# Kernel optimization log

Hardware: AMD Instinct MI355X
Metric: run time of the kernel (lower is better)

## Reference

```python
import jax, jax.numpy as jnp
import numpy as np

N_HEADS = 4
D_K = 32
C = 128
SCALE = D_K ** (-0.5)


def setup_inputs() -> dict:
    key = jax.random.key(0)
    k1, k2, k3, k4, k5 = jax.random.split(key, 5)
    x = jax.random.normal(k1, (16, C, 32, 32), dtype=jnp.float32)
    # nn.Linear(C, n_heads*d_k*3): weight [out, in], bias [out]
    Wp = jax.random.normal(k2, (N_HEADS * D_K * 3, C), dtype=jnp.float32) * (C ** -0.5)
    bp = jax.random.normal(k3, (N_HEADS * D_K * 3,), dtype=jnp.float32) * 0.01
    # nn.Linear(n_heads*d_k, C)
    Wo = jax.random.normal(k4, (C, N_HEADS * D_K), dtype=jnp.float32) * ((N_HEADS * D_K) ** -0.5)
    bo = jax.random.normal(k5, (C,), dtype=jnp.float32) * 0.01
    return {"x": x, "Wp": Wp, "bp": bp, "Wo": Wo, "bo": bo}


def reference(x, Wp, bp, Wo, bo):
    b, c, h, w = x.shape
    n = h * w
    # (b,c,h,w) -> (b, n, c); NOTE: GroupNorm from __init__ is never applied in forward.
    xf = x.reshape(b, c, n).transpose(0, 2, 1)
    qkv = (xf @ Wp.T + bp).reshape(b, n, N_HEADS, 3 * D_K)
    q, k, v = jnp.split(qkv, 3, axis=-1)  # each (b, n, heads, d_k)
    attn = jnp.einsum('bihd,bjhd->bijh', q, k) * SCALE  # (b, n, n, heads)
    # Faithful to original: softmax over LAST axis = heads axis (original code bug)
    attn = jax.nn.softmax(attn, axis=-1)
    res = jnp.einsum('bijh,bjhd->bihd', attn, v).reshape(b, n, N_HEADS * D_K)
    res = res @ Wo.T + bo + xf
    return res.transpose(0, 2, 1).reshape(b, c, h, w)
```

## Files before the change

### kernel.cpp

```cpp
#include <hip/hip_runtime.h>

typedef short s8v __attribute__((ext_vector_type(8)));
typedef float f4v __attribute__((ext_vector_type(4)));

#define NTOK 1024
#define CD 128
#define QSCALE 0.25506953149031838f

__device__ __forceinline__ ushort f2bf(float x) {
    union { float f; unsigned u; } v; v.f = x;
    unsigned u = v.u + 0x7fff + ((v.u >> 16) & 1);
    return (ushort)(u >> 16);
}
__device__ __forceinline__ float bf2f(ushort x) {
    union { unsigned u; float f; } v; v.u = ((unsigned)x) << 16;
    return v.f;
}
__device__ __forceinline__ void gl_lds16(const ushort* g, ushort* l) {
    __builtin_amdgcn_global_load_lds(
        (const __attribute__((address_space(1))) unsigned int*)(g),
        (__attribute__((address_space(3))) unsigned int*)(l), 16, 0, 0);
}
__device__ __forceinline__ unsigned cvt_pk_bf16(float lo, float hi) {
    unsigned r;
    asm("v_cvt_pk_bf16_f32 %0, %1, %2" : "=v"(r) : "v"(lo), "v"(hi));
    return r;
}

__global__ __launch_bounds__(256) void k_pre(const float* __restrict__ x,
                                             const float* __restrict__ Wp,
                                             const float* __restrict__ Wo,
                                             ushort* __restrict__ xt,
                                             ushort* __restrict__ wpre) {
    const int t = threadIdx.x;
    const int bx = blockIdx.x;
    if (bx < 256) {
        __shared__ ushort tile[128 * 68];
        const int b = bx >> 4;
        const int n0 = (bx & 15) << 6;
        #pragma unroll
        for (int p = 0; p < 8; ++p) {
            const int c = p * 16 + (t >> 4);
            const int n4 = t & 15;
            const float4 v = *(const float4*)&x[(b * CD + c) * NTOK + n0 + n4 * 4];
            ushort4 o;
            o.x = f2bf(v.x); o.y = f2bf(v.y); o.z = f2bf(v.z); o.w = f2bf(v.w);
            *(ushort4*)&tile[c * 68 + n4 * 4] = o;
        }
        __syncthreads();
        #pragma unroll
        for (int p = 0; p < 4; ++p) {
            const int nl = t >> 2;
            const int g = (t & 3) + p * 4;
            s8v tmp;
            #pragma unroll
            for (int e = 0; e < 8; ++e) tmp[e] = (short)tile[(g * 8 + e) * 68 + nl];
            const int n = n0 + nl;
            *(s8v*)&xt[(b * NTOK + n) * CD + ((g ^ (nl & 7)) * 8)] = tmp;
        }
    } else {
        const int kind = bx - 256;
        ushort* dst = wpre + kind * (CD * CD);
        for (int e = t * 4; e < CD * CD; e += 1024) {
            const int f = e >> 7, c = e & 127;
            const float* src;
            if (kind == 3) src = &Wo[f * CD + c];
            else           src = &Wp[((f >> 5) * 96 + kind * 32 + (f & 31)) * CD + c];
            const float4 v = *(const float4*)src;
            ushort4 o;
            o.x = f2bf(v.x); o.y = f2bf(v.y); o.z = f2bf(v.z); o.w = f2bf(v.w);
            *(ushort4*)&dst[f * CD + (((c >> 3) ^ (f & 7)) * 8) + (c & 7)] = o;
        }
    }
}

__global__ __launch_bounds__(256) void k_proj(const ushort* __restrict__ xt,
                                              const ushort* __restrict__ wpre,
                                              const float* __restrict__ bp,
                                              ushort* __restrict__ qb,
                                              ushort* __restrict__ kb,
                                              ushort* __restrict__ vtb) {
    __shared__ ushort Abuf[128 * 128];
    __shared__ ushort Bbuf[64 * 128];
    const int t = threadIdx.x;
    const int lane = t & 63;
    const int w = t >> 6;
    const int li = lane & 15;
    const int lg = lane >> 4;
    const int bx = blockIdx.x;
    const int kind = bx >> 8;
    const int idx = bx & 255;

    const ushort* Asrc;
    const ushort* Bsrc;
    if (kind < 2) {
        Asrc = xt + (idx >> 1) * 128 * CD;
        Bsrc = wpre + kind * (CD * CD) + (idx & 1) * 64 * CD;
    } else {
        Asrc = wpre + 2 * (CD * CD);
        Bsrc = xt + idx * 64 * CD;
    }
    {
        const ushort* ga = Asrc + w * 4096;
        ushort* la = Abuf + w * 4096;
        #pragma unroll
        for (int i = 0; i < 8; ++i) gl_lds16(ga + i * 512 + lane * 8, la + i * 512);
        const ushort* gb = Bsrc + w * 2048;
        ushort* lb = Bbuf + w * 2048;
        #pragma unroll
        for (int i = 0; i < 4; ++i) gl_lds16(gb + i * 512 + lane * 8, lb + i * 512);
    }
    __syncthreads();

    const f4v fz = {0.f, 0.f, 0.f, 0.f};
    f4v acc[2][4];
    #pragma unroll
    for (int mf = 0; mf < 2; ++mf)
        #pragma unroll
        for (int nf = 0; nf < 4; ++nf) acc[mf][nf] = fz;
    const int m_base = w * 32;
    #pragma unroll
    for (int kk = 0; kk < 4; ++kk) {
        s8v a[2], bb[4];
        #pragma unroll
        for (int mf = 0; mf < 2; ++mf) {
            const int row = m_base + mf * 16 + li;
            a[mf] = *(const s8v*)&Abuf[row * CD + (((kk * 4 + lg) ^ (row & 7)) * 8)];
        }
        #pragma unroll
        for (int nf = 0; nf < 4; ++nf) {
            const int row = nf * 16 + li;
            bb[nf] = *(const s8v*)&Bbuf[row * CD + (((kk * 4 + lg) ^ (row & 7)) * 8)];
        }
        #pragma unroll
        for (int mf = 0; mf < 2; ++mf)
            #pragma unroll
            for (int nf = 0; nf < 4; ++nf)
                acc[mf][nf] = __builtin_amdgcn_mfma_f32_16x16x32_bf16(a[mf], bb[nf], acc[mf][nf], 0, 0, 0);
    }

    if (kind < 2) {
        ushort* dst = (kind == 0) ? qb : kb;
        const int m0 = (idx >> 1) * 128;
        const int f0 = (idx & 1) * 64;
        #pragma unroll
        for (int mf = 0; mf < 2; ++mf)
            #pragma unroll
            for (int nf = 0; nf < 4; ++nf) {
                const int f = f0 + nf * 16 + li;
                const int o = (f >> 5) * 96 + kind * 32 + (f & 31);
                const float bias = bp[o];
                #pragma unroll
                for (int r = 0; r < 4; ++r) {
                    const int row = m0 + m_base + mf * 16 + lg * 4 + r;
                    float v = acc[mf][nf][r] + bias;
                    if (kind == 0) v *= QSCALE;
                    dst[row * CD + f] = f2bf(v);
                }
            }
    } else {
        const int n0g = idx * 64;
        const int b = n0g >> 10;
        const int nl0 = n0g & 1023;
        #pragma unroll
        for (int mf = 0; mf < 2; ++mf)
            #pragma unroll
            for (int r = 0; r < 4; ++r) {
                const int f = m_base + mf * 16 + lg * 4 + r;
                const int o = (f >> 5) * 96 + 64 + (f & 31);
                const float bias = bp[o];
                #pragma unroll
                for (int nf = 0; nf < 4; ++nf) {
                    const int n = nl0 + nf * 16 + li;
                    const int jl = n & 31;
                    const int np = (n & ~31) | (((jl & 15) >> 2) * 8 + (jl & 3) + ((jl >> 4) << 2));
                    vtb[(b * CD + f) * NTOK + np] = f2bf(acc[mf][nf][r] + bias);
                }
            }
    }
}

__global__ __launch_bounds__(256) void k_attn(const ushort* __restrict__ qb,
                                              const ushort* __restrict__ kb,
                                              const ushort* __restrict__ vtb,
                                              ushort* __restrict__ res4) {
    __shared__ ushort kbuf[2][32 * 136];
    __shared__ ushort vbuf[2][128 * 40];
    const int t = threadIdx.x;
    const int lane = t & 63;
    const int w = t >> 6;
    const int b = blockIdx.x;
    const int it = blockIdx.y;
    const int js = blockIdx.z;
    const int i0 = it * 64 + w * 16;
    const int li = lane & 15;
    const int lg = lane >> 4;

    s8v qf[4];
    #pragma unroll
    for (int h = 0; h < 4; ++h)
        qf[h] = *(const s8v*)&qb[(b*NTOK + i0 + li)*CD + h*32 + lg*8];

    const f4v fz = {0.f, 0.f, 0.f, 0.f};
    f4v acc[4][2];
    #pragma unroll
    for (int h = 0; h < 4; ++h) { acc[h][0] = fz; acc[h][1] = fz; }

    const int j0 = js * 256;
    const ushort* kptr0 = &kb[(b*NTOK + j0 + (t>>4))*CD + (t&15)*8];
    const ushort* kptr1 = kptr0 + 16*CD;
    const ushort* vptr0 = &vtb[(b*CD + (t>>2))*NTOK + j0 + (t&3)*8];
    const ushort* vptr1 = vptr0 + 64*NTOK;
    const int kwo = (t>>4)*136 + (t&15)*8;
    const int vwo = (t>>2)*40 + (t&3)*8;

    s8v k0 = *(const s8v*)kptr0;
    s8v k1 = *(const s8v*)kptr1;
    s8v v0 = *(const s8v*)vptr0;
    s8v v1 = *(const s8v*)vptr1;
    *(s8v*)&kbuf[0][kwo]          = k0;
    *(s8v*)&kbuf[0][kwo + 16*136] = k1;
    *(s8v*)&vbuf[0][vwo]          = v0;
    *(s8v*)&vbuf[0][vwo + 64*40]  = v1;
    k0 = *(const s8v*)(kptr0 + 32*CD);
    k1 = *(const s8v*)(kptr1 + 32*CD);
    v0 = *(const s8v*)(vptr0 + 32);
    v1 = *(const s8v*)(vptr1 + 32);
    __syncthreads();

    unsigned wv[4][4];
    {
        f4v sv[4][2];
        __builtin_amdgcn_s_setprio(1);
        #pragma unroll
        for (int h = 0; h < 4; ++h)
            #pragma unroll
            for (int jh = 0; jh < 2; ++jh) {
                s8v kf = *(const s8v*)&kbuf[0][(jh*16 + li)*136 + h*32 + lg*8];
                sv[h][jh] = __builtin_amdgcn_mfma_f32_16x16x32_bf16(kf, qf[h], fz, 0, 0, 0);
            }
        __builtin_amdgcn_s_setprio(0);
        #pragma unroll
        for (int jh = 0; jh < 2; ++jh)
            #pragma unroll
            for (int r = 0; r < 4; ++r) {
                float e0 = __builtin_amdgcn_exp2f(sv[0][jh][r]);
                float e1 = __builtin_amdgcn_exp2f(sv[1][jh][r]);
                float e2 = __builtin_amdgcn_exp2f(sv[2][jh][r]);
                float e3 = __builtin_amdgcn_exp2f(sv[3][jh][r]);
                float inv = __builtin_amdgcn_rcpf(e0 + e1 + e2 + e3);
                sv[0][jh][r] = e0 * inv;
                sv[1][jh][r] = e1 * inv;
                sv[2][jh][r] = e2 * inv;
                sv[3][jh][r] = e3 * inv;
            }
        #pragma unroll
        for (int h = 0; h < 4; ++h) {
            wv[h][0] = cvt_pk_bf16(sv[h][0][0], sv[h][0][1]);
            wv[h][1] = cvt_pk_bf16(sv[h][0][2], sv[h][0][3]);
            wv[h][2] = cvt_pk_bf16(sv[h][1][0], sv[h][1][1]);
            wv[h][3] = cvt_pk_bf16(sv[h][1][2], sv[h][1][3]);
        }
    }

    #pragma unroll
    for (int tt = 1; tt <= 8; ++tt) {
        if (tt <= 7) {
            ushort* kn = kbuf[tt & 1];
            *(s8v*)&kn[kwo]          = k0;
            *(s8v*)&kn[kwo + 16*136] = k1;
        }
        __syncthreads();
        if (tt <= 7) {
            ushort* vn = vbuf[tt & 1];
            *(s8v*)&vn[vwo]          = v0;
            *(s8v*)&vn[vwo + 64*40]  = v1;
        }
        if (tt <= 6) {
            k0 = *(const s8v*)(kptr0 + (tt+1)*32*CD);
            k1 = *(const s8v*)(kptr1 + (tt+1)*32*CD);
            v0 = *(const s8v*)(vptr0 + (tt+1)*32);
            v1 = *(const s8v*)(vptr1 + (tt+1)*32);
        }
        f4v sv[4][2];
        if (tt <= 7) {
            const ushort* kc = kbuf[tt & 1];
            __builtin_amdgcn_s_setprio(1);
            #pragma unroll
            for (int h = 0; h < 4; ++h)
                #pragma unroll
                for (int jh = 0; jh < 2; ++jh) {
                    s8v kf = *(const s8v*)&kc[(jh*16 + li)*136 + h*32 + lg*8];
                    sv[h][jh] = __builtin_amdgcn_mfma_f32_16x16x32_bf16(kf, qf[h], fz, 0, 0, 0);
                }
            __builtin_amdgcn_s_setprio(0);
        }
        {
            const ushort* vc = vbuf[(tt - 1) & 1];
            #pragma unroll
            for (int h = 0; h < 4; ++h) {
                union { unsigned d[4]; s8v s; } av;
                av.d[0] = wv[h][0]; av.d[1] = wv[h][1];
                av.d[2] = wv[h][2]; av.d[3] = wv[h][3];
                s8v vf0 = *(const s8v*)&vc[(h*32 + li)*40 + lg*8];
                s8v vf1 = *(const s8v*)&vc[(h*32 + 16 + li)*40 + lg*8];
                __builtin_amdgcn_s_setprio(1);
                acc[h][0] = __builtin_amdgcn_mfma_f32_16x16x32_bf16(av.s, vf0, acc[h][0], 0, 0, 0);
                acc[h][1] = __builtin_amdgcn_mfma_f32_16x16x32_bf16(av.s, vf1, acc[h][1], 0, 0, 0);
                __builtin_amdgcn_s_setprio(0);
            }
        }
        if (tt <= 7) {
            #pragma unroll
            for (int jh = 0; jh < 2; ++jh)
                #pragma unroll
                for (int r = 0; r < 4; ++r) {
                    float e0 = __builtin_amdgcn_exp2f(sv[0][jh][r]);
                    float e1 = __builtin_amdgcn_exp2f(sv[1][jh][r]);
                    float e2 = __builtin_amdgcn_exp2f(sv[2][jh][r]);
                    float e3 = __builtin_amdgcn_exp2f(sv[3][jh][r]);
                    float inv = __builtin_amdgcn_rcpf(e0 + e1 + e2 + e3);
                    sv[0][jh][r] = e0 * inv;
                    sv[1][jh][r] = e1 * inv;
                    sv[2][jh][r] = e2 * inv;
                    sv[3][jh][r] = e3 * inv;
                }
            #pragma unroll
            for (int h = 0; h < 4; ++h) {
                wv[h][0] = cvt_pk_bf16(sv[h][0][0], sv[h][0][1]);
                wv[h][1] = cvt_pk_bf16(sv[h][0][2], sv[h][0][3]);
                wv[h][2] = cvt_pk_bf16(sv[h][1][0], sv[h][1][1]);
                wv[h][3] = cvt_pk_bf16(sv[h][1][2], sv[h][1][3]);
            }
        }
    }

    #pragma unroll
    for (int h = 0; h < 4; ++h)
        #pragma unroll
        for (int dh = 0; dh < 2; ++dh)
            #pragma unroll
            for (int r = 0; r < 4; ++r) {
                const int i = i0 + lg*4 + r;
                const int f = h*32 + dh*16 + li;
                res4[js*(16*NTOK*CD) + (b*NTOK + i)*CD + f] = f2bf(acc[h][dh][r]);
            }
}

__global__ __launch_bounds__(256) void k_out(const ushort* __restrict__ wpre,
                                             const ushort* __restrict__ res4,
                                             const float* __restrict__ bo,
                                             const float* __restrict__ x,
                                             float* __restrict__ out) {
    __shared__ ushort Abuf[128 * 128];
    __shared__ ushort Bbuf[64 * 128];
    const int t = threadIdx.x;
    const int lane = t & 63;
    const int w = t >> 6;
    const int li = lane & 15;
    const int lg = lane >> 4;
    const int idx = blockIdx.x;
    const int n0g = idx * 64;
    const int b = n0g >> 10;
    {
        const ushort* ga = wpre + 3 * (CD * CD) + w * 4096;
        ushort* la = Abuf + w * 4096;
        #pragma unroll
        for (int i = 0; i < 8; ++i) gl_lds16(ga + i * 512 + lane * 8, la + i * 512);
    }
    for (int u = t; u < 64 * 16; u += 256) {
        const int rl = u >> 4, g = u & 15;
        const ushort* p = &res4[(n0g + rl) * CD + g * 8];
        s8v p0 = *(const s8v*)(p);
        s8v p1 = *(const s8v*)(p + 16*NTOK*CD);
        s8v p2 = *(const s8v*)(p + 32*NTOK*CD);
        s8v p3 = *(const s8v*)(p + 48*NTOK*CD);
        s8v sm;
        #pragma unroll
        for (int e = 0; e < 8; ++e)
            sm[e] = (short)f2bf(bf2f((ushort)p0[e]) + bf2f((ushort)p1[e])
                              + bf2f((ushort)p2[e]) + bf2f((ushort)p3[e]));
        *(s8v*)&Bbuf[rl * CD + ((g ^ (rl & 7)) * 8)] = sm;
    }
    __syncthreads();

    const f4v fz = {0.f, 0.f, 0.f, 0.f};
    f4v acc[2][4];
    #pragma unroll
    for (int mf = 0; mf < 2; ++mf)
        #pragma unroll
        for (int nf = 0; nf < 4; ++nf) acc[mf][nf] = fz;
    const int m_base = w * 32;
    #pragma unroll
    for (int kk = 0; kk < 4; ++kk) {
        s8v a[2], bb[4];
        #pragma unroll
        for (int mf = 0; mf < 2; ++mf) {
            const int row = m_base + mf * 16 + li;
            a[mf] = *(const s8v*)&Abuf[row * CD + (((kk * 4 + lg) ^ (row & 7)) * 8)];
        }
        #pragma unroll
        for (int nf = 0; nf < 4; ++nf) {
            const int row = nf * 16 + li;
            bb[nf] = *(const s8v*)&Bbuf[row * CD + (((kk * 4 + lg) ^ (row & 7)) * 8)];
        }
        #pragma unroll
        for (int mf = 0; mf < 2; ++mf)
            #pragma unroll
            for (int nf = 0; nf < 4; ++nf)
                acc[mf][nf] = __builtin_amdgcn_mfma_f32_16x16x32_bf16(a[mf], bb[nf], acc[mf][nf], 0, 0, 0);
    }
    const int nl0 = n0g & 1023;
    #pragma unroll
    for (int mf = 0; mf < 2; ++mf)
        #pragma unroll
        for (int r = 0; r < 4; ++r) {
            const int o = m_base + mf * 16 + lg * 4 + r;
            const float bias = bo[o];
            #pragma unroll
            for (int nf = 0; nf < 4; ++nf) {
                const int n = nl0 + nf * 16 + li;
                const int gi = (b * CD + o) * NTOK + n;
                out[gi] = acc[mf][nf][r] + bias + x[gi];
            }
        }
}

extern "C" void kernel_launch(void* const* d_in, const int* in_sizes, int n_in,
                              void* d_out, int out_size, void* d_ws, size_t ws_size,
                              hipStream_t stream) {
    const float* x  = (const float*)d_in[0];
    const float* Wp = (const float*)d_in[1];
    const float* bp = (const float*)d_in[2];
    const float* Wo = (const float*)d_in[3];
    const float* bo = (const float*)d_in[4];
    float* out = (float*)d_out;
    ushort* xt   = (ushort*)d_ws;
    ushort* wpre = xt + 16*1024*128;
    ushort* qbw  = wpre + 4*128*128;
    ushort* kbw  = qbw + 16*1024*128;
    ushort* vtb  = kbw + 16*1024*128;
    ushort* res4 = vtb + 16*1024*128;
    k_pre <<<260, 256, 0, stream>>>(x, Wp, Wo, xt, wpre);
    k_proj<<<768, 256, 0, stream>>>(xt, wpre, bp, qbw, kbw, vtb);
    k_attn<<<dim3(16, 16, 4), 256, 0, stream>>>(qbw, kbw, vtb, res4);
    k_out <<<256, 256, 0, stream>>>(wpre, res4, bo, x, out);
}
```

Baseline: 49.34 us.

## Widen projection tiles to full feature width and double attention block size

The Q/K projection blocks now compute all 128 output features per 128-token tile, so each block loads the x tile once instead of two blocks each loading it. The grid shrinks from 768 to 512 blocks. The attention kernel moves to 512-thread blocks covering 128 query rows, so each K/V tile staged in shared memory is shared by twice as many query rows and each thread loads half as much. This trades fewer blocks and more registers and LDS per block for less redundant global traffic.

```diff
diff --git a/kernel.cpp b/kernel.cpp
--- a/kernel.cpp
+++ b/kernel.cpp
@@ -81,73 +81,64 @@
                                               ushort* __restrict__ kb,
                                               ushort* __restrict__ vtb) {
     __shared__ ushort Abuf[128 * 128];
-    __shared__ ushort Bbuf[64 * 128];
+    __shared__ ushort Bbuf[128 * 128];
     const int t = threadIdx.x;
     const int lane = t & 63;
     const int w = t >> 6;
     const int li = lane & 15;
     const int lg = lane >> 4;
     const int bx = blockIdx.x;
-    const int kind = bx >> 8;
-    const int idx = bx & 255;
-
-    const ushort* Asrc;
-    const ushort* Bsrc;
-    if (kind < 2) {
-        Asrc = xt + (idx >> 1) * 128 * CD;
-        Bsrc = wpre + kind * (CD * CD) + (idx & 1) * 64 * CD;
-    } else {
-        Asrc = wpre + 2 * (CD * CD);
-        Bsrc = xt + idx * 64 * CD;
-    }
-    {
-        const ushort* ga = Asrc + w * 4096;
-        ushort* la = Abuf + w * 4096;
-        #pragma unroll
-        for (int i = 0; i < 8; ++i) gl_lds16(ga + i * 512 + lane * 8, la + i * 512);
-        const ushort* gb = Bsrc + w * 2048;
-        ushort* lb = Bbuf + w * 2048;
-        #pragma unroll
-        for (int i = 0; i < 4; ++i) gl_lds16(gb + i * 512 + lane * 8, lb + i * 512);
-    }
-    __syncthreads();
-
     const f4v fz = {0.f, 0.f, 0.f, 0.f};
-    f4v acc[2][4];
-    #pragma unroll
-    for (int mf = 0; mf < 2; ++mf)
-        #pragma unroll
-        for (int nf = 0; nf < 4; ++nf) acc[mf][nf] = fz;
     const int m_base = w * 32;
-    #pragma unroll
-    for (int kk = 0; kk < 4; ++kk) {
-        s8v a[2], bb[4];
-        #pragma unroll
-        for (int mf = 0; mf < 2; ++mf) {
-            const int row = m_base + mf * 16 + li;
-            a[mf] = *(const s8v*)&Abuf[row * CD + (((kk * 4 + lg) ^ (row & 7)) * 8)];
-        }
-        #pragma unroll
-        for (int nf = 0; nf < 4; ++nf) {
-            const int row = nf * 16 + li;
-            bb[nf] = *(const s8v*)&Bbuf[row * CD + (((kk * 4 + lg) ^ (row & 7)) * 8)];
-        }
+
+    if (bx < 256) {
+        const int kind = bx >> 7;
+        const int idx = bx & 127;
+        const ushort* Asrc = xt + idx * 128 * CD;
+        const ushort* Bsrc = wpre + kind * (CD * CD);
+        {
+            const ushort* ga = Asrc + w * 4096;
+            ushort* la = Abuf + w * 4096;
+            #pragma unroll
+            for (int i = 0; i < 8; ++i) gl_lds16(ga + i * 512 + lane * 8, la + i * 512);
+            const ushort* gb = Bsrc + w * 4096;
+            ushort* lb = Bbuf + w * 4096;
+            #pragma unroll
+            for (int i = 0; i < 8; ++i) gl_lds16(gb + i * 512 + lane * 8, lb + i * 512);
+        }
+        __syncthreads();
+
+        f4v acc[2][8];
         #pragma unroll
         for (int mf = 0; mf < 2; ++mf)
             #pragma unroll
-            for (int nf = 0; nf < 4; ++nf)
-                acc[mf][nf] = __builtin_amdgcn_mfma_f32_16x16x32_bf16(a[mf], bb[nf], acc[mf][nf], 0, 0, 0);
-    }
-
-    if (kind < 2) {
+            for (int nf = 0; nf < 8; ++nf) acc[mf][nf] = fz;
+        #pragma unroll
+        for (int kk = 0; kk < 4; ++kk) {
+            s8v a[2], bb[8];
+            #pragma unroll
+            for (int mf = 0; mf < 2; ++mf) {
+                const int row = m_base + mf * 16 + li;
+                a[mf] = *(const s8v*)&Abuf[row * CD + (((kk * 4 + lg) ^ (row & 7)) * 8)];
+            }
+            #pragma unroll
+            for (int nf = 0; nf < 8; ++nf) {
+                const int row = nf * 16 + li;
+                bb[nf] = *(const s8v*)&Bbuf[row * CD + (((kk * 4 + lg) ^ (row & 7)) * 8)];
+            }
+            #pragma unroll
+            for (int mf = 0; mf < 2; ++mf)
+                #pragma unroll
+                for (int nf = 0; nf < 8; ++nf)
+                    acc[mf][nf] = __builtin_amdgcn_mfma_f32_16x16x32_bf16(a[mf], bb[nf], acc[mf][nf], 0, 0, 0);
+        }
         ushort* dst = (kind == 0) ? qb : kb;
-        const int m0 = (idx >> 1) * 128;
-        const int f0 = (idx & 1) * 64;
+        const int m0 = idx * 128;
         #pragma unroll
         for (int mf = 0; mf < 2; ++mf)
             #pragma unroll
-            for (int nf = 0; nf < 4; ++nf) {
-                const int f = f0 + nf * 16 + li;
+            for (int nf = 0; nf < 8; ++nf) {
+                const int f = nf * 16 + li;
                 const int o = (f >> 5) * 96 + kind * 32 + (f & 31);
                 const float bias = bp[o];
                 #pragma unroll
@@ -159,6 +150,45 @@
                 }
             }
     } else {
+        const int idx = bx - 256;
+        const ushort* Asrc = wpre + 2 * (CD * CD);
+        const ushort* Bsrc = xt + idx * 64 * CD;
+        {
+            const ushort* ga = Asrc + w * 4096;
+            ushort* la = Abuf + w * 4096;
+            #pragma unroll
+            for (int i = 0; i < 8; ++i) gl_lds16(ga + i * 512 + lane * 8, la + i * 512);
+            const ushort* gb = Bsrc + w * 2048;
+            ushort* lb = Bbuf + w * 2048;
+            #pragma unroll
+            for (int i = 0; i < 4; ++i) gl_lds16(gb + i * 512 + lane * 8, lb + i * 512);
+        }
+        __syncthreads();
+
+        f4v acc[2][4];
+        #pragma unroll
+        for (int mf = 0; mf < 2; ++mf)
+            #pragma unroll
+            for (int nf = 0; nf < 4; ++nf) acc[mf][nf] = fz;
+        #pragma unroll
+        for (int kk = 0; kk < 4; ++kk) {
+            s8v a[2], bb[4];
+            #pragma unroll
+            for (int mf = 0; mf < 2; ++mf) {
+                const int row = m_base + mf * 16 + li;
+                a[mf] = *(const s8v*)&Abuf[row * CD + (((kk * 4 + lg) ^ (row & 7)) * 8)];
+            }
+            #pragma unroll
+            for (int nf = 0; nf < 4; ++nf) {
+                const int row = nf * 16 + li;
+                bb[nf] = *(const s8v*)&Bbuf[row * CD + (((kk * 4 + lg) ^ (row & 7)) * 8)];
+            }
+            #pragma unroll
+            for (int mf = 0; mf < 2; ++mf)
+                #pragma unroll
+                for (int nf = 0; nf < 4; ++nf)
+                    acc[mf][nf] = __builtin_amdgcn_mfma_f32_16x16x32_bf16(a[mf], bb[nf], acc[mf][nf], 0, 0, 0);
+        }
         const int n0g = idx * 64;
         const int b = n0g >> 10;
         const int nl0 = n0g & 1023;
@@ -180,7 +210,7 @@
     }
 }
 
-__global__ __launch_bounds__(256) void k_attn(const ushort* __restrict__ qb,
+__global__ __launch_bounds__(512) void k_attn(const ushort* __restrict__ qb,
                                               const ushort* __restrict__ kb,
                                               const ushort* __restrict__ vtb,
                                               ushort* __restrict__ res4) {
@@ -192,7 +222,7 @@
     const int b = blockIdx.x;
     const int it = blockIdx.y;
     const int js = blockIdx.z;
-    const int i0 = it * 64 + w * 16;
+    const int i0 = it * 128 + w * 16;
     const int li = lane & 15;
     const int lg = lane >> 4;
 
@@ -208,24 +238,16 @@
 
     const int j0 = js * 256;
     const ushort* kptr0 = &kb[(b*NTOK + j0 + (t>>4))*CD + (t&15)*8];
-    const ushort* kptr1 = kptr0 + 16*CD;
     const ushort* vptr0 = &vtb[(b*CD + (t>>2))*NTOK + j0 + (t&3)*8];
-    const ushort* vptr1 = vptr0 + 64*NTOK;
     const int kwo = (t>>4)*136 + (t&15)*8;
     const int vwo = (t>>2)*40 + (t&3)*8;
 
     s8v k0 = *(const s8v*)kptr0;
-    s8v k1 = *(const s8v*)kptr1;
     s8v v0 = *(const s8v*)vptr0;
-    s8v v1 = *(const s8v*)vptr1;
-    *(s8v*)&kbuf[0][kwo]          = k0;
-    *(s8v*)&kbuf[0][kwo + 16*136] = k1;
-    *(s8v*)&vbuf[0][vwo]          = v0;
-    *(s8v*)&vbuf[0][vwo + 64*40]  = v1;
+    *(s8v*)&kbuf[0][kwo] = k0;
+    *(s8v*)&vbuf[0][vwo] = v0;
     k0 = *(const s8v*)(kptr0 + 32*CD);
-    k1 = *(const s8v*)(kptr1 + 32*CD);
     v0 = *(const s8v*)(vptr0 + 32);
-    v1 = *(const s8v*)(vptr1 + 32);
     __syncthreads();
 
     unsigned wv[4][4];
@@ -266,21 +288,15 @@
     #pragma unroll
     for (int tt = 1; tt <= 8; ++tt) {
         if (tt <= 7) {
-            ushort* kn = kbuf[tt & 1];
-            *(s8v*)&kn[kwo]          = k0;
-            *(s8v*)&kn[kwo + 16*136] = k1;
+            *(s8v*)&kbuf[tt & 1][kwo] = k0;
         }
         __syncthreads();
         if (tt <= 7) {
-            ushort* vn = vbuf[tt & 1];
-            *(s8v*)&vn[vwo]          = v0;
-            *(s8v*)&vn[vwo + 64*40]  = v1;
+            *(s8v*)&vbuf[tt & 1][vwo] = v0;
         }
         if (tt <= 6) {
             k0 = *(const s8v*)(kptr0 + (tt+1)*32*CD);
-            k1 = *(const s8v*)(kptr1 + (tt+1)*32*CD);
             v0 = *(const s8v*)(vptr0 + (tt+1)*32);
-            v1 = *(const s8v*)(vptr1 + (tt+1)*32);
         }
         f4v sv[4][2];
         if (tt <= 7) {
@@ -442,7 +458,7 @@
     ushort* vtb  = kbw + 16*1024*128;
     ushort* res4 = vtb + 16*1024*128;
     k_pre <<<260, 256, 0, stream>>>(x, Wp, Wo, xt, wpre);
-    k_proj<<<768, 256, 0, stream>>>(xt, wpre, bp, qbw, kbw, vtb);
-    k_attn<<<dim3(16, 16, 4), 256, 0, stream>>>(qbw, kbw, vtb, res4);
+    k_proj<<<512, 256, 0, stream>>>(xt, wpre, bp, qbw, kbw, vtb);
+    k_attn<<<dim3(16, 8, 4), 512, 0, stream>>>(qbw, kbw, vtb, res4);
     k_out <<<256, 256, 0, stream>>>(wpre, res4, bo, x, out);
 }
```

Measured after the change: 49.69 us. Within noise of the previous version (+0.7%).
